# Optimization experiments

Measured on AMD Instinct MI355X. Metric: run time of the kernel, lower is better.

## Reference

```python
import jax, jax.numpy as jnp
import numpy as np

NUM_FREQS = 12  # fourfeat_config
EMB_DIM = 3 + 6 * NUM_FREQS  # identity + sin/cos per freq per dim = 75


def fourier_ipe(x, cov, decay):
    # x: [N,3], cov: [N,3,3], decay: scalar (coarse-to-fine window cutoff)
    N = x.shape[0]
    freqs = 2.0 ** jnp.arange(NUM_FREQS, dtype=jnp.float32)            # [F]
    xb = x[:, None, :] * freqs[:, None]                                # [N,F,3]
    var = jnp.diagonal(cov, axis1=-2, axis2=-1)[:, None, :] * (freqs ** 2)[:, None]  # [N,F,3]
    # nerfies-style cosine easing window per frequency band
    window = 0.5 * (1.0 - jnp.cos(jnp.pi * jnp.clip(decay - jnp.arange(NUM_FREQS, dtype=jnp.float32), 0.0, 1.0)))  # [F]
    atten = jnp.exp(-0.5 * var) * window[:, None]                      # [N,F,3]
    four = jnp.concatenate([jnp.sin(xb), jnp.cos(xb)], axis=-1) * jnp.concatenate([atten, atten], axis=-1)  # [N,F,6]
    return jnp.concatenate([x, four.reshape(N, 6 * NUM_FREQS)], axis=-1)  # [N,75]


def mlp(h, W_in, b_in, W_hid, b_hid, W_out, b_out):
    h = jax.nn.relu(h @ W_in + b_in)
    for i in range(W_hid.shape[0]):  # fixed small layer count
        h = jax.nn.relu(h @ W_hid[i] + b_hid[i])
    return h @ W_out + b_out  # output_activation = None


def setup_inputs() -> dict:
    key = jax.random.key(0)
    ks = jax.random.split(key, 16)
    bshape = (2, 16384, 8)
    mean = jax.random.normal(ks[0], (*bshape, 3), jnp.float32)
    cov = jax.random.uniform(ks[1], (*bshape, 3, 3), jnp.float32) * 1e-4  # small positive diag

    def w(k, shp):
        return jax.random.normal(k, shp, jnp.float32) / np.sqrt(shp[-2]).astype(np.float32)

    FD, FC = 256, 128  # features_density, features_color
    HD, HC = 8 - 2, 4 - 2  # n_hidden_layers = layers - 2
    return {
        'mean': mean, 'cov': cov,
        'Wd_in': w(ks[2], (EMB_DIM, FD)), 'bd_in': jnp.zeros((FD,), jnp.float32),
        'Wd_hid': w(ks[3], (HD, FD, FD)), 'bd_hid': jnp.zeros((HD, FD), jnp.float32),
        'Wd_out': w(ks[4], (FD, FD + 1)), 'bd_out': jnp.zeros((FD + 1,), jnp.float32),
        'Wc_in': w(ks[5], (FD, FC)), 'bc_in': jnp.zeros((FC,), jnp.float32),
        'Wc_hid': w(ks[6], (HC, FC, FC)), 'bc_hid': jnp.zeros((HC, FC), jnp.float32),
        'Wc_out': w(ks[7], (FC, 3)), 'bc_out': jnp.zeros((3,), jnp.float32),
        'decayscale': 12,
    }


def reference(mean, cov, Wd_in, bd_in, Wd_hid, bd_hid, Wd_out, bd_out,
              Wc_in, bc_in, Wc_hid, bc_hid, Wc_out, bc_out, decayscale):
    batch_shape = mean.shape[:-1]
    N = int(np.prod(batch_shape))
    x = mean.reshape(N, 3)
    c = cov.reshape(N, 3, 3)
    emb = fourier_ipe(x, c, jnp.float32(decayscale))                    # [N,75]
    feat = mlp(emb, Wd_in, bd_in, Wd_hid, bd_hid, Wd_out, bd_out)       # [N,257]
    d, features = feat[:, :1], feat[:, 1:]
    # parameterization == 'VolSDF' (capitalized) -> no SDF radius offset branch
    raw_rgb = mlp(features, Wc_in, bc_in, Wc_hid, bc_hid, Wc_out, bc_out)  # [N,3]
    raw = jnp.concatenate([raw_rgb, d], axis=-1)                        # [N,4]
    return raw.reshape(*batch_shape, 4)
```

## Files before the change

kernel.cpp:

```cpp
#include <hip/hip_runtime.h>
#include <hip/hip_bf16.h>

#define PI_F 3.14159265358979323846f
#define KPAD 260

typedef _Float16 h8 __attribute__((ext_vector_type(8)));
typedef _Float16 h4 __attribute__((ext_vector_type(4)));
typedef float f32x16 __attribute__((ext_vector_type(16)));

#define OFF_DIN   0
#define OFF_DHID  24576
#define OFF_DOUT  417792
#define OFF_CIN   516096
#define OFF_CHID  548864
#define OFF_COUT  581632
#define W_TOTAL   585728
#define B_DIN  0
#define B_DHID 256
#define B_FEAT 1792
#define B_CIN  2176
#define B_CHID 2304
#define B_TOTAL 2560
#define PREP_TOTAL (W_TOTAL + B_TOTAL)

__global__ void prep_kernel(const float* __restrict__ Wd_in,  const float* __restrict__ Wd_hid,
                            const float* __restrict__ Wd_out, const float* __restrict__ Wc_in,
                            const float* __restrict__ Wc_hid, const float* __restrict__ Wc_out,
                            const float* __restrict__ bd_in,  const float* __restrict__ bd_hid,
                            const float* __restrict__ bd_out, const float* __restrict__ bc_in,
                            const float* __restrict__ bc_hid,
                            _Float16* __restrict__ wdst, float* __restrict__ bdst)
{
    int i = blockIdx.x * 256 + threadIdx.x;
    if (i >= PREP_TOTAL) return;
    if (i < W_TOTAL) {
        float v = 0.f;
        int j, KT, n, k;
        #define DECODE(jj, KTv)  do { int frag = (jj) >> 3; int e = (jj) & 7;          \
                                      int lane = frag & 63; int tk = frag >> 6;         \
                                      int ntl = tk / (KTv); int kt = tk % (KTv);        \
                                      n = ntl * 32 + (lane & 31);                       \
                                      k = kt * 16 + (lane >> 5) * 8 + e; } while (0)
        if (i < OFF_DHID) {
            j = i; KT = 6; DECODE(j, KT);
            if (k < 75) v = Wd_in[k * 256 + n];
        } else if (i < OFF_DOUT) {
            j = i - OFF_DHID; int l = j >> 16; j &= 65535; KT = 16; DECODE(j, KT);
            v = Wd_hid[(l * 256 + k) * 256 + n];
        } else if (i < OFF_CIN) {
            j = i - OFF_DOUT; KT = 16; DECODE(j, KT);
            if (n < 256) v = Wd_out[k * 257 + n + 1];
            else if (n == 256) v = Wd_out[k * 257];
        } else if (i < OFF_CHID) {
            j = i - OFF_CIN; KT = 16; DECODE(j, KT);
            v = Wc_in[k * 128 + n];
        } else if (i < OFF_COUT) {
            j = i - OFF_CHID; int l = j >> 14; j &= 16383; KT = 8; DECODE(j, KT);
            v = Wc_hid[(l * 128 + k) * 128 + n];
        } else {
            j = i - OFF_COUT; KT = 8; DECODE(j, KT);
            if (n < 3) v = Wc_out[k * 3 + n];
        }
        #undef DECODE
        wdst[i] = (_Float16)v;
    } else {
        int b = i - W_TOTAL;
        float v = 0.f;
        if (b < B_DHID)      v = bd_in[b];
        else if (b < B_FEAT) v = bd_hid[b - B_DHID];
        else if (b < B_CIN)  { int n = b - B_FEAT;
                               if (n < 256) v = bd_out[n + 1]; else if (n == 256) v = bd_out[0]; }
        else if (b < B_CHID) v = bc_in[b - B_CIN];
        else                 v = bc_hid[b - B_CHID];
        bdst[b] = v;
    }
}

__device__ __forceinline__ h8 lds_read_h8(const _Float16* p)
{
    h4 lo = *(const h4*)(p);
    h4 hi = *(const h4*)(p + 4);
    return __builtin_shufflevector(lo, hi, 0, 1, 2, 3, 4, 5, 6, 7);
}

template<int KT, int NT, bool RELU, bool GUARD>
__device__ __forceinline__ void dense(_Float16 (*At)[KPAD],
                                      const _Float16* __restrict__ WP,
                                      const float* __restrict__ bias,
                                      int rbase, int ntile0, int lrow, int lq, int lane,
                                      float* dval)
{
    f32x16 acc[2][NT];
#pragma unroll
    for (int mt = 0; mt < 2; ++mt)
#pragma unroll
        for (int nt = 0; nt < NT; ++nt)
#pragma unroll
            for (int j = 0; j < 16; ++j) acc[mt][nt][j] = 0.f;

    const _Float16* wbase = WP + ((size_t)ntile0 * KT) * 512 + (size_t)lane * 8;

#pragma unroll 2
    for (int kt = 0; kt < KT; ++kt) {
        const int koff = kt * 16 + lq * 8;
        h8 wf[NT];
#pragma unroll
        for (int nt = 0; nt < NT; ++nt)
            wf[nt] = *(const h8*)(wbase + (size_t)(nt * KT + kt) * 512);
        h8 af[2];
#pragma unroll
        for (int mt = 0; mt < 2; ++mt)
            af[mt] = lds_read_h8(&At[rbase + mt * 32 + lrow][koff]);
#pragma unroll
        for (int mt = 0; mt < 2; ++mt)
#pragma unroll
            for (int nt = 0; nt < NT; ++nt)
                acc[mt][nt] = __builtin_amdgcn_mfma_f32_32x32x16_f16(wf[nt], af[mt], acc[mt][nt], 0, 0, 0);
    }

    __syncthreads();

#pragma unroll
    for (int mt = 0; mt < 2; ++mt) {
        const int m = rbase + mt * 32 + lrow;
#pragma unroll
        for (int nt = 0; nt < NT; ++nt) {
#pragma unroll
            for (int p = 0; p < 4; ++p) {
                const int n0 = (ntile0 + nt) * 32 + p * 8 + lq * 4;
                if (GUARD && n0 >= 256) {
                    if (n0 == 256) dval[m] = acc[mt][nt][4 * p] + bias[256];
                } else {
                    float4 bv = *(const float4*)(bias + n0);
                    float a0 = acc[mt][nt][4 * p + 0] + bv.x;
                    float a1 = acc[mt][nt][4 * p + 1] + bv.y;
                    float a2 = acc[mt][nt][4 * p + 2] + bv.z;
                    float a3 = acc[mt][nt][4 * p + 3] + bv.w;
                    if (RELU) {
                        a0 = fmaxf(a0, 0.f); a1 = fmaxf(a1, 0.f);
                        a2 = fmaxf(a2, 0.f); a3 = fmaxf(a3, 0.f);
                    }
                    h4 hv;
                    hv[0] = (_Float16)a0; hv[1] = (_Float16)a1;
                    hv[2] = (_Float16)a2; hv[3] = (_Float16)a3;
                    *(h4*)(&At[m][n0]) = hv;
                }
            }
        }
    }
    __syncthreads();
}

__global__ __launch_bounds__(512, 4)
void ffmlp_kernel(const float* __restrict__ mean, const float* __restrict__ cov,
                  const int* __restrict__ decayscale,
                  const _Float16* __restrict__ wws, const float* __restrict__ bws,
                  const float* __restrict__ bc_out,
                  float* __restrict__ out, int N)
{
    __shared__ __align__(16) _Float16 At[128][KPAD];
    __shared__ float dval[128];

    const int t = threadIdx.x;
    const int wid = t >> 6, lane = t & 63;
    const int c = wid & 3, r = wid >> 2;
    const int lrow = lane & 31, lq = lane >> 5;
    const int rbase = r * 64;
    const int p0 = blockIdx.x * 128;

    {
        const int m = t >> 2, q = t & 3;
        const long pt = (long)p0 + m;
        float x0 = 0.f, x1 = 0.f, x2 = 0.f, v0 = 0.f, v1 = 0.f, v2 = 0.f;
        if (pt < N) {
            x0 = mean[pt * 3 + 0]; x1 = mean[pt * 3 + 1]; x2 = mean[pt * 3 + 2];
            v0 = cov[pt * 9 + 0];  v1 = cov[pt * 9 + 4];  v2 = cov[pt * 9 + 8];
        }
        const float dec = (float)(*decayscale);
        if (q == 0) {
            At[m][0] = (_Float16)x0; At[m][1] = (_Float16)x1; At[m][2] = (_Float16)x2;
            for (int k = 75; k < 80; ++k) At[m][k] = (_Float16)0.f;
        } else {
            for (int k = 75 + 5 * q; k < (q == 3 ? 96 : 80 + 5 * q); ++k) At[m][k] = (_Float16)0.f;
        }
        const float xs[3] = {x0, x1, x2}, vs[3] = {v0, v1, v2};
#pragma unroll
        for (int fi = 0; fi < 3; ++fi) {
            const int f = q * 3 + fi;
            const float fs = (float)(1 << f);
            const float wcl = fminf(fmaxf(dec - (float)f, 0.f), 1.f);
            const float win = 0.5f * (1.f - cosf(wcl * PI_F));
#pragma unroll
            for (int d = 0; d < 3; ++d) {
                const float xb = xs[d] * fs;
                const float att = expf(-0.5f * vs[d] * fs * fs) * win;
                float s, co;
                sincosf(xb, &s, &co);
                At[m][3 + 6 * f + d] = (_Float16)(s * att);
                At[m][6 + 6 * f + d] = (_Float16)(co * att);
            }
        }
    }
    __syncthreads();

    dense<6, 2, true, false>(At, wws + OFF_DIN, bws + B_DIN, rbase, c * 2, lrow, lq, lane, dval);
#pragma unroll 1
    for (int i = 0; i < 6; ++i)
        dense<16, 2, true, false>(At, wws + OFF_DHID + i * 65536, bws + B_DHID + i * 256,
                                  rbase, c * 2, lrow, lq, lane, dval);
    dense<16, 3, false, true>(At, wws + OFF_DOUT, bws + B_FEAT, rbase, c * 3, lrow, lq, lane, dval);

    dense<16, 1, true, false>(At, wws + OFF_CIN, bws + B_CIN, rbase, c, lrow, lq, lane, dval);
#pragma unroll 1
    for (int i = 0; i < 2; ++i)
        dense<8, 1, true, false>(At, wws + OFF_CHID + i * 16384, bws + B_CHID + i * 128,
                                 rbase, c, lrow, lq, lane, dval);

    if (c == 0) {
        f32x16 acc[2];
#pragma unroll
        for (int mt = 0; mt < 2; ++mt)
#pragma unroll
            for (int j = 0; j < 16; ++j) acc[mt][j] = 0.f;
        const _Float16* wco = wws + OFF_COUT + (size_t)lane * 8;
#pragma unroll
        for (int kt = 0; kt < 8; ++kt) {
            const int koff = kt * 16 + lq * 8;
            h8 wf = *(const h8*)(wco + (size_t)kt * 512);
#pragma unroll
            for (int mt = 0; mt < 2; ++mt) {
                h8 af = lds_read_h8(&At[rbase + mt * 32 + lrow][koff]);
                acc[mt] = __builtin_amdgcn_mfma_f32_32x32x16_f16(wf, af, acc[mt], 0, 0, 0);
            }
        }
        const float bc0 = bc_out[0], bc1 = bc_out[1], bc2 = bc_out[2];
        if (lq == 0) {
#pragma unroll
            for (int mt = 0; mt < 2; ++mt) {
                const int m = rbase + mt * 32 + lrow;
                const long pt = (long)p0 + m;
                if (pt < N) {
                    float4 o;
                    o.x = acc[mt][0] + bc0;
                    o.y = acc[mt][1] + bc1;
                    o.z = acc[mt][2] + bc2;
                    o.w = dval[m];
                    *(float4*)(out + pt * 4) = o;
                }
            }
        }
    }
}

extern "C" void kernel_launch(void* const* d_in, const int* in_sizes, int n_in,
                              void* d_out, int out_size, void* d_ws, size_t ws_size,
                              hipStream_t stream)
{
    const float* mean   = (const float*)d_in[0];
    const float* cov    = (const float*)d_in[1];
    const float* Wd_in  = (const float*)d_in[2];
    const float* bd_in  = (const float*)d_in[3];
    const float* Wd_hid = (const float*)d_in[4];
    const float* bd_hid = (const float*)d_in[5];
    const float* Wd_out = (const float*)d_in[6];
    const float* bd_out = (const float*)d_in[7];
    const float* Wc_in  = (const float*)d_in[8];
    const float* bc_in  = (const float*)d_in[9];
    const float* Wc_hid = (const float*)d_in[10];
    const float* bc_hid = (const float*)d_in[11];
    const float* Wc_out = (const float*)d_in[12];
    const float* bc_out = (const float*)d_in[13];
    const int*   decay  = (const int*)d_in[14];

    _Float16* wws = (_Float16*)d_ws;
    float*    bws = (float*)((char*)d_ws + (size_t)W_TOTAL * 2);

    const int N = in_sizes[0] / 3;

    const int prep_blocks = (PREP_TOTAL + 255) / 256;
    prep_kernel<<<prep_blocks, 256, 0, stream>>>(Wd_in, Wd_hid, Wd_out, Wc_in, Wc_hid, Wc_out,
                                                 bd_in, bd_hid, bd_out, bc_in, bc_hid, wws, bws);

    const int blocks = (N + 127) / 128;
    ffmlp_kernel<<<blocks, 512, 0, stream>>>(mean, cov, decay, wws, bws, bc_out, (float*)d_out, N);
}
```

Before: 326.0 us.

## Shrink blocks to 64 rows, preload bias into accumulators, compute density via dot

Halves the block size to 256 threads and 64 points so each block runs four waves over one row group. Biases are stored in MFMA fragment order and loaded as the initial accumulator, and the epilogue uses packed fp16 conversion with a vector ReLU. The extra 257th density output column is dropped from the output GEMM and replaced by a per-wave partial dot product over the previous activations, reduced through shared memory. MFMA issue is wrapped in s_setprio. The trade-off is that each weight fragment fetched from global/L2 is now reused across only 64 rows instead of 128.

New measurement: 315.1 us. 3.3% less time.

```diff
diff --git a/kernel.cpp b/kernel.cpp
--- a/kernel.cpp
+++ b/kernel.cpp
@@ -6,21 +6,31 @@
 
 typedef _Float16 h8 __attribute__((ext_vector_type(8)));
 typedef _Float16 h4 __attribute__((ext_vector_type(4)));
+typedef _Float16 h2 __attribute__((ext_vector_type(2)));
+typedef __fp16 fp16x2 __attribute__((ext_vector_type(2)));
 typedef float f32x16 __attribute__((ext_vector_type(16)));
+
+__device__ __forceinline__ h2 cvt_pk_h2(float a, float b)
+{
+    fp16x2 r = __builtin_amdgcn_cvt_pkrtz(a, b);
+    return __builtin_bit_cast(h2, r);
+}
 
 #define OFF_DIN   0
 #define OFF_DHID  24576
-#define OFF_DOUT  417792
-#define OFF_CIN   516096
-#define OFF_CHID  548864
-#define OFF_COUT  581632
-#define W_TOTAL   585728
-#define B_DIN  0
-#define B_DHID 256
-#define B_FEAT 1792
-#define B_CIN  2176
-#define B_CHID 2304
-#define B_TOTAL 2560
+#define OFF_FEAT  417792
+#define OFF_CIN   483328
+#define OFF_CHID  516096
+#define OFF_COUT  548864
+#define W_TOTAL   552960
+#define FB_DIN  0
+#define FB_DHID 256
+#define FB_FEAT 1792
+#define FB_CIN  2048
+#define FB_CHID 2176
+#define FB_WD0  2432
+#define FB_BD0  2688
+#define B_TOTAL 2689
 #define PREP_TOTAL (W_TOTAL + B_TOTAL)
 
 __global__ void prep_kernel(const float* __restrict__ Wd_in,  const float* __restrict__ Wd_hid,
@@ -35,30 +45,29 @@
     if (i >= PREP_TOTAL) return;
     if (i < W_TOTAL) {
         float v = 0.f;
-        int j, KT, n, k;
+        int j, n, k;
         #define DECODE(jj, KTv)  do { int frag = (jj) >> 3; int e = (jj) & 7;          \
                                       int lane = frag & 63; int tk = frag >> 6;         \
                                       int ntl = tk / (KTv); int kt = tk % (KTv);        \
                                       n = ntl * 32 + (lane & 31);                       \
                                       k = kt * 16 + (lane >> 5) * 8 + e; } while (0)
         if (i < OFF_DHID) {
-            j = i; KT = 6; DECODE(j, KT);
+            j = i; DECODE(j, 6);
             if (k < 75) v = Wd_in[k * 256 + n];
-        } else if (i < OFF_DOUT) {
-            j = i - OFF_DHID; int l = j >> 16; j &= 65535; KT = 16; DECODE(j, KT);
+        } else if (i < OFF_FEAT) {
+            j = i - OFF_DHID; int l = j >> 16; j &= 65535; DECODE(j, 16);
             v = Wd_hid[(l * 256 + k) * 256 + n];
         } else if (i < OFF_CIN) {
-            j = i - OFF_DOUT; KT = 16; DECODE(j, KT);
-            if (n < 256) v = Wd_out[k * 257 + n + 1];
-            else if (n == 256) v = Wd_out[k * 257];
+            j = i - OFF_FEAT; DECODE(j, 16);
+            v = Wd_out[k * 257 + n + 1];
         } else if (i < OFF_CHID) {
-            j = i - OFF_CIN; KT = 16; DECODE(j, KT);
+            j = i - OFF_CIN; DECODE(j, 16);
             v = Wc_in[k * 128 + n];
         } else if (i < OFF_COUT) {
-            j = i - OFF_CHID; int l = j >> 14; j &= 16383; KT = 8; DECODE(j, KT);
+            j = i - OFF_CHID; int l = j >> 14; j &= 16383; DECODE(j, 8);
             v = Wc_hid[(l * 128 + k) * 128 + n];
         } else {
-            j = i - OFF_COUT; KT = 8; DECODE(j, KT);
+            j = i - OFF_COUT; DECODE(j, 8);
             if (n < 3) v = Wc_out[k * 3 + n];
         }
         #undef DECODE
@@ -66,12 +75,19 @@
     } else {
         int b = i - W_TOTAL;
         float v = 0.f;
-        if (b < B_DHID)      v = bd_in[b];
-        else if (b < B_FEAT) v = bd_hid[b - B_DHID];
-        else if (b < B_CIN)  { int n = b - B_FEAT;
-                               if (n < 256) v = bd_out[n + 1]; else if (n == 256) v = bd_out[0]; }
-        else if (b < B_CHID) v = bc_in[b - B_CIN];
-        else                 v = bc_hid[b - B_CHID];
+        #define BDECODE(bb) int ntl = (bb) >> 5; int r5 = (bb) & 31;                   \
+                            int lq = r5 >> 4, jj = r5 & 15;                            \
+                            int n = ntl * 32 + (jj & 3) + 8 * (jj >> 2) + 4 * lq
+        if (b < FB_DHID)      { BDECODE(b); v = bd_in[n]; }
+        else if (b < FB_FEAT) { int b2 = b - FB_DHID; int l = b2 >> 8; int bb = b2 & 255;
+                                BDECODE(bb); v = bd_hid[l * 256 + n]; }
+        else if (b < FB_CIN)  { int bb = b - FB_FEAT; BDECODE(bb); v = bd_out[n + 1]; }
+        else if (b < FB_CHID) { int bb = b - FB_CIN; BDECODE(bb); v = bc_in[n]; }
+        else if (b < FB_WD0)  { int b2 = b - FB_CHID; int l = b2 >> 7; int bb = b2 & 127;
+                                BDECODE(bb); v = bc_hid[l * 128 + n]; }
+        else if (b < FB_BD0)  { int k = b - FB_WD0; v = Wd_out[k * 257]; }
+        else                  { v = bd_out[0]; }
+        #undef BDECODE
         bdst[b] = v;
     }
 }
@@ -83,20 +99,22 @@
     return __builtin_shufflevector(lo, hi, 0, 1, 2, 3, 4, 5, 6, 7);
 }
 
-template<int KT, int NT, bool RELU, bool GUARD>
+template<int KT, int NT, bool RELU, bool DDOT>
 __device__ __forceinline__ void dense(_Float16 (*At)[KPAD],
                                       const _Float16* __restrict__ WP,
-                                      const float* __restrict__ bias,
-                                      int rbase, int ntile0, int lrow, int lq, int lane,
-                                      float* dval)
-{
+                                      const float* __restrict__ bfrag,
+                                      const float* __restrict__ wd0,
+                                      float (*dpart)[64],
+                                      int c, int lrow, int lq, int lane)
+{
+    const int ntile0 = c * NT;
     f32x16 acc[2][NT];
 #pragma unroll
-    for (int mt = 0; mt < 2; ++mt)
-#pragma unroll
-        for (int nt = 0; nt < NT; ++nt)
-#pragma unroll
-            for (int j = 0; j < 16; ++j) acc[mt][nt][j] = 0.f;
+    for (int nt = 0; nt < NT; ++nt) {
+        f32x16 b = *(const f32x16*)(bfrag + (ntile0 + nt) * 32 + lq * 16);
+        acc[0][nt] = b;
+        acc[1][nt] = b;
+    }
 
     const _Float16* wbase = WP + ((size_t)ntile0 * KT) * 512 + (size_t)lane * 8;
 
@@ -110,63 +128,67 @@
         h8 af[2];
 #pragma unroll
         for (int mt = 0; mt < 2; ++mt)
-            af[mt] = lds_read_h8(&At[rbase + mt * 32 + lrow][koff]);
+            af[mt] = lds_read_h8(&At[mt * 32 + lrow][koff]);
+        __builtin_amdgcn_s_setprio(1);
 #pragma unroll
         for (int mt = 0; mt < 2; ++mt)
 #pragma unroll
             for (int nt = 0; nt < NT; ++nt)
                 acc[mt][nt] = __builtin_amdgcn_mfma_f32_32x32x16_f16(wf[nt], af[mt], acc[mt][nt], 0, 0, 0);
+        __builtin_amdgcn_s_setprio(0);
+    }
+
+    if (DDOT) {
+        float s = 0.f;
+        const float* w0 = wd0 + c * 64;
+#pragma unroll
+        for (int kk = 0; kk < 64; kk += 8) {
+            h8 hv = lds_read_h8(&At[lane][c * 64 + kk]);
+#pragma unroll
+            for (int e = 0; e < 8; ++e)
+                s = fmaf((float)hv[e], w0[kk + e], s);
+        }
+        dpart[c][lane] = s;
     }
 
     __syncthreads();
 
 #pragma unroll
     for (int mt = 0; mt < 2; ++mt) {
-        const int m = rbase + mt * 32 + lrow;
+        const int m = mt * 32 + lrow;
 #pragma unroll
         for (int nt = 0; nt < NT; ++nt) {
 #pragma unroll
             for (int p = 0; p < 4; ++p) {
                 const int n0 = (ntile0 + nt) * 32 + p * 8 + lq * 4;
-                if (GUARD && n0 >= 256) {
-                    if (n0 == 256) dval[m] = acc[mt][nt][4 * p] + bias[256];
-                } else {
-                    float4 bv = *(const float4*)(bias + n0);
-                    float a0 = acc[mt][nt][4 * p + 0] + bv.x;
-                    float a1 = acc[mt][nt][4 * p + 1] + bv.y;
-                    float a2 = acc[mt][nt][4 * p + 2] + bv.z;
-                    float a3 = acc[mt][nt][4 * p + 3] + bv.w;
-                    if (RELU) {
-                        a0 = fmaxf(a0, 0.f); a1 = fmaxf(a1, 0.f);
-                        a2 = fmaxf(a2, 0.f); a3 = fmaxf(a3, 0.f);
-                    }
-                    h4 hv;
-                    hv[0] = (_Float16)a0; hv[1] = (_Float16)a1;
-                    hv[2] = (_Float16)a2; hv[3] = (_Float16)a3;
-                    *(h4*)(&At[m][n0]) = hv;
+                h2 lo = cvt_pk_h2(acc[mt][nt][4 * p + 0], acc[mt][nt][4 * p + 1]);
+                h2 hi = cvt_pk_h2(acc[mt][nt][4 * p + 2], acc[mt][nt][4 * p + 3]);
+                h4 hv = __builtin_shufflevector(lo, hi, 0, 1, 2, 3);
+                if (RELU) {
+                    const h4 zero = {(_Float16)0, (_Float16)0, (_Float16)0, (_Float16)0};
+                    hv = __builtin_elementwise_max(hv, zero);
                 }
+                *(h4*)(&At[m][n0]) = hv;
             }
         }
     }
     __syncthreads();
 }
 
-__global__ __launch_bounds__(512, 4)
+__global__ __launch_bounds__(256, 4)
 void ffmlp_kernel(const float* __restrict__ mean, const float* __restrict__ cov,
                   const int* __restrict__ decayscale,
                   const _Float16* __restrict__ wws, const float* __restrict__ bws,
                   const float* __restrict__ bc_out,
                   float* __restrict__ out, int N)
 {
-    __shared__ __align__(16) _Float16 At[128][KPAD];
-    __shared__ float dval[128];
+    __shared__ __align__(16) _Float16 At[64][KPAD];
+    __shared__ float dpart[4][64];
 
     const int t = threadIdx.x;
-    const int wid = t >> 6, lane = t & 63;
-    const int c = wid & 3, r = wid >> 2;
+    const int c = t >> 6, lane = t & 63;
     const int lrow = lane & 31, lq = lane >> 5;
-    const int rbase = r * 64;
-    const int p0 = blockIdx.x * 128;
+    const int p0 = blockIdx.x * 64;
 
     {
         const int m = t >> 2, q = t & 3;
@@ -203,18 +225,18 @@
     }
     __syncthreads();
 
-    dense<6, 2, true, false>(At, wws + OFF_DIN, bws + B_DIN, rbase, c * 2, lrow, lq, lane, dval);
+    dense<6, 2, true, false>(At, wws + OFF_DIN, bws + FB_DIN, bws, dpart, c, lrow, lq, lane);
 #pragma unroll 1
     for (int i = 0; i < 6; ++i)
-        dense<16, 2, true, false>(At, wws + OFF_DHID + i * 65536, bws + B_DHID + i * 256,
-                                  rbase, c * 2, lrow, lq, lane, dval);
-    dense<16, 3, false, true>(At, wws + OFF_DOUT, bws + B_FEAT, rbase, c * 3, lrow, lq, lane, dval);
-
-    dense<16, 1, true, false>(At, wws + OFF_CIN, bws + B_CIN, rbase, c, lrow, lq, lane, dval);
+        dense<16, 2, true, false>(At, wws + OFF_DHID + i * 65536, bws + FB_DHID + i * 256,
+                                  bws, dpart, c, lrow, lq, lane);
+    dense<16, 2, false, true>(At, wws + OFF_FEAT, bws + FB_FEAT, bws + FB_WD0, dpart, c, lrow, lq, lane);
+
+    dense<16, 1, true, false>(At, wws + OFF_CIN, bws + FB_CIN, bws, dpart, c, lrow, lq, lane);
 #pragma unroll 1
     for (int i = 0; i < 2; ++i)
-        dense<8, 1, true, false>(At, wws + OFF_CHID + i * 16384, bws + B_CHID + i * 128,
-                                 rbase, c, lrow, lq, lane, dval);
+        dense<8, 1, true, false>(At, wws + OFF_CHID + i * 16384, bws + FB_CHID + i * 128,
+                                 bws, dpart, c, lrow, lq, lane);
 
     if (c == 0) {
         f32x16 acc[2];
@@ -229,22 +251,23 @@
             h8 wf = *(const h8*)(wco + (size_t)kt * 512);
 #pragma unroll
             for (int mt = 0; mt < 2; ++mt) {
-                h8 af = lds_read_h8(&At[rbase + mt * 32 + lrow][koff]);
+                h8 af = lds_read_h8(&At[mt * 32 + lrow][koff]);
                 acc[mt] = __builtin_amdgcn_mfma_f32_32x32x16_f16(wf, af, acc[mt], 0, 0, 0);
             }
         }
         const float bc0 = bc_out[0], bc1 = bc_out[1], bc2 = bc_out[2];
+        const float bd0 = bws[FB_BD0];
         if (lq == 0) {
 #pragma unroll
             for (int mt = 0; mt < 2; ++mt) {
-                const int m = rbase + mt * 32 + lrow;
+                const int m = mt * 32 + lrow;
                 const long pt = (long)p0 + m;
                 if (pt < N) {
                     float4 o;
                     o.x = acc[mt][0] + bc0;
                     o.y = acc[mt][1] + bc1;
                     o.z = acc[mt][2] + bc2;
-                    o.w = dval[m];
+                    o.w = dpart[0][m] + dpart[1][m] + dpart[2][m] + dpart[3][m] + bd0;
                     *(float4*)(out + pt * 4) = o;
                 }
             }
@@ -281,6 +304,6 @@
     prep_kernel<<<prep_blocks, 256, 0, stream>>>(Wd_in, Wd_hid, Wd_out, Wc_in, Wc_hid, Wc_out,
                                                  bd_in, bd_hid, bd_out, bc_in, bc_hid, wws, bws);
 
-    const int blocks = (N + 127) / 128;
-    ffmlp_kernel<<<blocks, 512, 0, stream>>>(mean, cov, decay, wws, bws, bc_out, (float*)d_out, N);
-}
+    const int blocks = (N + 63) / 64;
+    ffmlp_kernel<<<blocks, 256, 0, stream>>>(mean, cov, decay, wws, bws, bc_out, (float*)d_out, N);
+}
```
